# Kernel tuning notes

Hardware: AMD Instinct MI355X
Metric: run time of the kernel (lower is better)

Reference implementation:

```python
import jax, jax.numpy as jnp
import numpy as np

B, N, S, VC, P, E, H = 8, 1024, 64, 8, 3, 64, 4
HD = E // H


def setup_inputs() -> dict:
    key = jax.random.key(0)
    ks = jax.random.split(key, 20)
    def rn(k, shape, scale=1.0):
        return jax.random.normal(k, shape, dtype=jnp.float32) * scale
    inp = {
        "s": rn(ks[0], (B, N, S)),
        "v": rn(ks[1], (B, N, VC, 3)),
        "coords": rn(ks[2], (B, N, 3)),
        # p-adic encoder: Linear(1,16) -> SiLU -> Linear(16, 64)
        "enc_w1": rn(ks[3], (16, 1), 1.0),
        "enc_b1": jnp.zeros((16,), jnp.float32),
        "enc_w2": rn(ks[4], (S, 16), 1.0 / np.sqrt(16)),
        "enc_b2": jnp.zeros((S,), jnp.float32),
        # 3 GVP layers, all with s_cat dim 72 -> s_out 64, v 8 -> 8
        "scal_w": rn(ks[5], (3, S, S + VC), 1.0 / np.sqrt(S + VC)),
        "scal_b": jnp.zeros((3, S), jnp.float32),
        "vec_w": rn(ks[6], (3, VC, VC), 1.0 / np.sqrt(VC)),
        "gate_w": rn(ks[7], (3, VC, S + VC), 1.0 / np.sqrt(S + VC)),
        "gate_b": jnp.zeros((3, VC), jnp.float32),
        # MultiheadAttention (embed 64, 4 heads)
        "in_proj_w": rn(ks[8], (3 * E, E), 1.0 / np.sqrt(E)),
        "in_proj_b": jnp.zeros((3 * E,), jnp.float32),
        "out_proj_w": rn(ks[9], (E, E), 1.0 / np.sqrt(E)),
        "out_proj_b": jnp.zeros((E,), jnp.float32),
    }
    return inp


def _padic_distance(coords):
    # pairwise diffs (B, N, N, 3)
    diff = coords[:, :, None, :] - coords[:, None, :, :]
    di = (jnp.abs(diff) * 1000.0).astype(jnp.int32)
    # valuation = max k in [1,10] with p^k | di  == count of divisible k (divisibility chain)
    cnt = jnp.zeros(di.shape, jnp.int32)
    for k in range(1, 11):
        cnt = cnt + (di % (P ** k) == 0).astype(jnp.int32)
    val = jnp.where(di > 0, cnt, 0).astype(jnp.float32).mean(-1)  # (B,N,N)
    return jnp.float32(P) ** (-val)


def reference(s, v, coords, enc_w1, enc_b1, enc_w2, enc_b2,
              scal_w, scal_b, vec_w, gate_w, gate_b,
              in_proj_w, in_proj_b, out_proj_w, out_proj_b):
    silu = jax.nn.silu
    pd = _padic_distance(coords)  # (B,N,N)
    pf = silu(pd.mean(-1, keepdims=True) @ enc_w1.T + enc_b1) @ enc_w2.T + enc_b2
    s = s + pf

    for i in range(3):
        act = i < 2  # last layer has no activations (gate always applied)
        vn = jnp.linalg.norm(v, axis=-1)               # (B,N,VC)
        sc = jnp.concatenate([s, vn], axis=-1)         # (B,N,S+VC)
        s_new = sc @ scal_w[i].T + scal_b[i]
        if act:
            s_new = silu(s_new)
        v_new = jnp.einsum('oi,bnix->bnox', vec_w[i], v)
        if act:
            v_new = v_new * jax.nn.sigmoid(jnp.linalg.norm(v_new, axis=-1, keepdims=True))
        gate = jax.nn.sigmoid(sc @ gate_w[i].T + gate_b[i])
        v_new = v_new * gate[..., None]
        if i > 0:
            s, v = s + s_new, v + v_new
        else:
            s, v = s_new, v_new

    # p-adic biased multi-head attention (additive mask = -padic_dist per head)
    qkv = s @ in_proj_w.T + in_proj_b                 # (B,N,3E)
    q, k, vv = jnp.split(qkv, 3, axis=-1)
    q = q.reshape(B, N, H, HD)
    k = k.reshape(B, N, H, HD)
    vv = vv.reshape(B, N, H, HD)
    scores = jnp.einsum('bqhd,bkhd->bhqk', q, k) / np.sqrt(HD)
    scores = scores - pd[:, None, :, :]
    attn = jax.nn.softmax(scores, axis=-1)
    o = jnp.einsum('bhqk,bkhd->bqhd', attn, vv).reshape(B, N, E)
    s = s + (o @ out_proj_w.T + out_proj_b)

    return s, v, pd
```

## Files before the change

### kernel.cpp

```cpp
#include <hip/hip_runtime.h>
#include <hip/hip_bf16.h>
#include <math.h>

#define BB 8
#define NN 1024
#define SS 64
#define VCC 8
#define EE 64
#define HH 4
#define HDD 16

#define OUT_S_OFF 0
#define OUT_V_OFF 524288
#define OUT_PD_OFF 720896

__device__ __forceinline__ int val3(int d) {
    int c = 0;
    unsigned ud = (unsigned)d;
    c += (ud % 3u == 0u);
    c += (ud % 9u == 0u);
    c += (ud % 27u == 0u);
    c += (ud % 81u == 0u);
    c += (ud % 243u == 0u);
    c += (ud % 729u == 0u);
    c += (ud % 2187u == 0u);
    c += (ud % 6561u == 0u);
    c += (ud % 19683u == 0u);
    c += (ud % 59049u == 0u);
    return d > 0 ? c : 0;
}

__device__ __forceinline__ float silu_f(float x) {
    return x / (1.0f + expf(-x));
}
__device__ __forceinline__ float sigmoid_f(float x) {
    return 1.0f / (1.0f + expf(-x));
}

__global__ __launch_bounds__(256) void pd_kernel(const float* __restrict__ coords,
                                                 float* __restrict__ pd_out,
                                                 float* __restrict__ pdmean) {
    const int row = blockIdx.x;
    const int b = row >> 10;
    const int i = row & 1023;
    const int tid = threadIdx.x;
    const float* cb = coords + (size_t)b * NN * 3;

    __shared__ float sx[1024];
    __shared__ float sy[1024];
    __shared__ float sz[1024];
    __shared__ float red[4];

    for (int idx = tid; idx < 3072; idx += 256) {
        float v = cb[idx];
        int j = idx / 3;
        int c = idx - j * 3;
        float* dst = (c == 0) ? sx : (c == 1) ? sy : sz;
        dst[j] = v;
    }
    __syncthreads();

    const float cx = sx[i], cy = sy[i], cz = sz[i];
    float* prow = pd_out + (size_t)row * NN;
    const float kLog2_3_over3 = 0.5283208335737187f;

    const int j0 = tid * 4;
    float4 x4 = *(const float4*)&sx[j0];
    float4 y4 = *(const float4*)&sy[j0];
    float4 z4 = *(const float4*)&sz[j0];

    float p[4];
    float xs[4] = {x4.x, x4.y, x4.z, x4.w};
    float ys[4] = {y4.x, y4.y, y4.z, y4.w};
    float zs[4] = {z4.x, z4.y, z4.z, z4.w};
    float lsum = 0.0f;
    #pragma unroll
    for (int t = 0; t < 4; ++t) {
        int d0 = (int)(fabsf(cx - xs[t]) * 1000.0f);
        int d1 = (int)(fabsf(cy - ys[t]) * 1000.0f);
        int d2 = (int)(fabsf(cz - zs[t]) * 1000.0f);
        int cnt = val3(d0) + val3(d1) + val3(d2);
        p[t] = exp2f(-(float)cnt * kLog2_3_over3);
        lsum += p[t];
    }
    float4 pv = make_float4(p[0], p[1], p[2], p[3]);
    *(float4*)&prow[j0] = pv;

    float x = lsum;
    #pragma unroll
    for (int off = 32; off > 0; off >>= 1) x += __shfl_xor(x, off, 64);
    if ((tid & 63) == 0) red[tid >> 6] = x;
    __syncthreads();
    if (tid == 0) pdmean[row] = (red[0] + red[1] + red[2] + red[3]) * (1.0f / 1024.0f);
}

#define GR 4
__global__ __launch_bounds__(64) void gvp_kernel(const float* __restrict__ s_in,
                           const float* __restrict__ v_in,
                           const float* __restrict__ enc_w1,
                           const float* __restrict__ enc_b1,
                           const float* __restrict__ enc_w2,
                           const float* __restrict__ enc_b2,
                           const float* __restrict__ scal_w,
                           const float* __restrict__ scal_b,
                           const float* __restrict__ vec_w,
                           const float* __restrict__ gate_w,
                           const float* __restrict__ gate_b,
                           const float* __restrict__ pdmean,
                           float* __restrict__ s_gvp,
                           float* __restrict__ v_out) {
    const int lane = threadIdx.x;
    const int rbase = blockIdx.x * GR;

    __shared__ float sc[GR][80];
    __shared__ float vbuf[GR][24];
    __shared__ float vtb[GR][24];
    __shared__ float gg[GR][8];
    __shared__ float hid[GR][16];

    #pragma unroll
    for (int r = 0; r < GR; ++r) {
        const int row = rbase + r;
        sc[r][lane] = s_in[(size_t)row * 64 + lane];
        if (lane < 24) vbuf[r][lane] = v_in[(size_t)row * 24 + lane];
        if (lane < 16) {
            float pm = pdmean[row];
            hid[r][lane] = silu_f(pm * enc_w1[lane] + enc_b1[lane]);
        }
    }
    __syncthreads();
    #pragma unroll
    for (int r = 0; r < GR; ++r) {
        float acc = enc_b2[lane];
        #pragma unroll
        for (int h = 0; h < 16; ++h) acc += hid[r][h] * enc_w2[lane * 16 + h];
        sc[r][lane] += acc;
    }
    __syncthreads();

    for (int layer = 0; layer < 3; ++layer) {
        const bool act = layer < 2;
        if (lane < 8) {
            #pragma unroll
            for (int r = 0; r < GR; ++r) {
                float x = vbuf[r][lane * 3 + 0];
                float y = vbuf[r][lane * 3 + 1];
                float z = vbuf[r][lane * 3 + 2];
                sc[r][64 + lane] = sqrtf(x * x + y * y + z * z);
            }
        }
        __syncthreads();

        float sn[GR];
        {
            float4 w4[18];
            const float4* wr = (const float4*)(scal_w + ((size_t)layer * 64 + lane) * 72);
            #pragma unroll
            for (int k = 0; k < 18; ++k) w4[k] = wr[k];
            const float sb = scal_b[layer * 64 + lane];
            #pragma unroll
            for (int r = 0; r < GR; ++r) {
                const float4* sv = (const float4*)sc[r];
                float acc = sb;
                #pragma unroll
                for (int k = 0; k < 18; ++k) {
                    float4 s4 = sv[k];
                    acc += w4[k].x * s4.x + w4[k].y * s4.y + w4[k].z * s4.z + w4[k].w * s4.w;
                }
                sn[r] = acc;
            }
        }
        if (lane < 8) {
            float4 g4[18];
            const float4* gr_ = (const float4*)(gate_w + ((size_t)layer * 8 + lane) * 72);
            #pragma unroll
            for (int k = 0; k < 18; ++k) g4[k] = gr_[k];
            const float gb = gate_b[layer * 8 + lane];
            #pragma unroll
            for (int r = 0; r < GR; ++r) {
                const float4* sv = (const float4*)sc[r];
                float acc = gb;
                #pragma unroll
                for (int k = 0; k < 18; ++k) {
                    float4 s4 = sv[k];
                    acc += g4[k].x * s4.x + g4[k].y * s4.y + g4[k].z * s4.z + g4[k].w * s4.w;
                }
                gg[r][lane] = sigmoid_f(acc);
            }
        }
        if (lane < 24) {
            const int o = lane / 3;
            const int xc = lane - o * 3;
            const float* vw = vec_w + ((size_t)layer * 8 + o) * 8;
            float vwr[8];
            #pragma unroll
            for (int ii = 0; ii < 8; ++ii) vwr[ii] = vw[ii];
            #pragma unroll
            for (int r = 0; r < GR; ++r) {
                float acc = 0.0f;
                #pragma unroll
                for (int ii = 0; ii < 8; ++ii) acc += vwr[ii] * vbuf[r][ii * 3 + xc];
                vtb[r][lane] = acc;
            }
        }
        __syncthreads();

        #pragma unroll
        for (int r = 0; r < GR; ++r) {
            float val = act ? silu_f(sn[r]) : sn[r];
            sc[r][lane] = (layer > 0) ? (sc[r][lane] + val) : val;
        }
        if (lane < 24) {
            const int o = lane / 3;
            #pragma unroll
            for (int r = 0; r < GR; ++r) {
                float val = vtb[r][lane];
                if (act) {
                    float a = vtb[r][o * 3 + 0];
                    float bb2 = vtb[r][o * 3 + 1];
                    float c2 = vtb[r][o * 3 + 2];
                    val *= sigmoid_f(sqrtf(a * a + bb2 * bb2 + c2 * c2));
                }
                val *= gg[r][o];
                vbuf[r][lane] = (layer > 0) ? (vbuf[r][lane] + val) : val;
            }
        }
        __syncthreads();
    }

    #pragma unroll
    for (int r = 0; r < GR; ++r) {
        const int row = rbase + r;
        s_gvp[(size_t)row * 64 + lane] = sc[r][lane];
        if (lane < 24) v_out[(size_t)row * 24 + lane] = vbuf[r][lane];
    }
}

#define QROWS 8
__global__ __launch_bounds__(192) void qkv_kernel(const float* __restrict__ s_gvp,
                           const float* __restrict__ w,
                           const float* __restrict__ bias,
                           float* __restrict__ q,
                           float* __restrict__ k,
                           float* __restrict__ v) {
    const int tid = threadIdx.x;
    const int rbase = blockIdx.x * QROWS;
    __shared__ float sl[QROWS][64];
    for (int idx = tid; idx < QROWS * 64; idx += 192)
        sl[idx >> 6][idx & 63] = s_gvp[(size_t)rbase * 64 + idx];
    __syncthreads();

    float4 w4[16];
    const float4* wr = (const float4*)(w + (size_t)tid * 64);
    #pragma unroll
    for (int kk = 0; kk < 16; ++kk) w4[kk] = wr[kk];
    const float bv = bias[tid];

    const int which = tid >> 6;
    const int e = tid & 63;
    const int h = e >> 4, d = e & 15;
    float* dst = (which == 0) ? q : (which == 1) ? k : v;

    #pragma unroll
    for (int r = 0; r < QROWS; ++r) {
        const float4* sv = (const float4*)sl[r];
        float acc = bv;
        #pragma unroll
        for (int kk = 0; kk < 16; ++kk) {
            float4 s4 = sv[kk];
            acc += w4[kk].x * s4.x + w4[kk].y * s4.y + w4[kk].z * s4.z + w4[kk].w * s4.w;
        }
        const int row = rbase + r;
        const int b = row >> 10, n = row & 1023;
        dst[(((size_t)(b * HH + h)) * NN + n) * HDD + d] = acc;
    }
}

__global__ __launch_bounds__(256, 2)
void attn_kernel(const float* __restrict__ q,
                 const float* __restrict__ k,
                 const float* __restrict__ v,
                 const float* __restrict__ pd,
                 float* __restrict__ o) {
    const int bh = blockIdx.x >> 5;
    const int qt = blockIdx.x & 31;
    const int b = bh >> 2;
    const int h = bh & 3;
    const int tid = threadIdx.x;
    const int kl = tid & 15;
    const int qg = tid >> 4;
    const int qbase = qt * 32 + qg * 2;

    __shared__ float kt[128][20];
    __shared__ float vt[128][20];

    float qreg[2][16];
    const float* qb_ = q + ((size_t)bh * NN + qbase) * HDD;
    #pragma unroll
    for (int i = 0; i < 2; ++i) {
        #pragma unroll
        for (int d = 0; d < 16; d += 4) {
            float4 t4 = *(const float4*)(qb_ + i * 16 + d);
            qreg[i][d] = t4.x; qreg[i][d+1] = t4.y; qreg[i][d+2] = t4.z; qreg[i][d+3] = t4.w;
        }
    }
    const float* pdr0 = pd + ((size_t)b * NN + qbase) * NN;

    float acc[2][16];
    #pragma unroll
    for (int i = 0; i < 2; ++i)
        #pragma unroll
        for (int d = 0; d < 16; ++d) acc[i][d] = 0.0f;
    float mrun[2] = {-INFINITY, -INFINITY};
    float lrun[2] = {0.0f, 0.0f};

    const float* kbase = k + (size_t)bh * NN * HDD;
    const float* vbase = v + (size_t)bh * NN * HDD;
    const float kLog2e = 1.44269504f;

    for (int tile = 0; tile < 8; ++tile) {
        __syncthreads();
        {
            const float4* kg = (const float4*)(kbase + (size_t)tile * 128 * 16);
            const float4* vg = (const float4*)(vbase + (size_t)tile * 128 * 16);
            int c0 = tid, c1 = tid + 256;
            int r0 = c0 >> 2, s0 = c0 & 3;
            int r1 = c1 >> 2, s1 = c1 & 3;
            *(float4*)&kt[r0][s0 * 4] = kg[c0];
            *(float4*)&kt[r1][s1 * 4] = kg[c1];
            *(float4*)&vt[r0][s0 * 4] = vg[c0];
            *(float4*)&vt[r1][s1 * 4] = vg[c1];
        }
        __syncthreads();

        float sc[2][8];
        #pragma unroll
        for (int m = 0; m < 8; ++m) {
            const int jt = kl + 16 * m;
            float kr[16];
            #pragma unroll
            for (int d = 0; d < 16; d += 4) {
                float4 t4 = *(const float4*)&kt[jt][d];
                kr[d] = t4.x; kr[d+1] = t4.y; kr[d+2] = t4.z; kr[d+3] = t4.w;
            }
            const int j = tile * 128 + jt;
            #pragma unroll
            for (int i = 0; i < 2; ++i) {
                float a = 0.0f;
                #pragma unroll
                for (int d = 0; d < 16; ++d) a += qreg[i][d] * kr[d];
                sc[i][m] = a * 0.25f - pdr0[(size_t)i * NN + j];
            }
        }

        #pragma unroll
        for (int i = 0; i < 2; ++i) {
            float tmax = sc[i][0];
            #pragma unroll
            for (int m = 1; m < 8; ++m) tmax = fmaxf(tmax, sc[i][m]);
            #pragma unroll
            for (int w = 1; w < 16; w <<= 1) tmax = fmaxf(tmax, __shfl_xor(tmax, w, 16));
            float mnew = fmaxf(mrun[i], tmax);
            float scale = exp2f((mrun[i] - mnew) * kLog2e);
            mrun[i] = mnew;
            lrun[i] *= scale;
            #pragma unroll
            for (int d = 0; d < 16; ++d) acc[i][d] *= scale;
            float ls = 0.0f;
            #pragma unroll
            for (int m = 0; m < 8; ++m) {
                float p = exp2f((sc[i][m] - mnew) * kLog2e);
                sc[i][m] = p;
                ls += p;
            }
            lrun[i] += ls;
        }

        #pragma unroll
        for (int m = 0; m < 8; ++m) {
            const int jt = kl + 16 * m;
            float vr[16];
            #pragma unroll
            for (int d = 0; d < 16; d += 4) {
                float4 t4 = *(const float4*)&vt[jt][d];
                vr[d] = t4.x; vr[d+1] = t4.y; vr[d+2] = t4.z; vr[d+3] = t4.w;
            }
            #pragma unroll
            for (int i = 0; i < 2; ++i) {
                const float p = sc[i][m];
                #pragma unroll
                for (int d = 0; d < 16; ++d) acc[i][d] += p * vr[d];
            }
        }
    }

    #pragma unroll
    for (int i = 0; i < 2; ++i) {
        float l = lrun[i];
        #pragma unroll
        for (int w = 1; w < 16; w <<= 1) l += __shfl_xor(l, w, 16);
        lrun[i] = l;
    }
    float outv[2] = {0.0f, 0.0f};
    #pragma unroll
    for (int i = 0; i < 2; ++i) {
        #pragma unroll
        for (int d = 0; d < 16; ++d) {
            float a = acc[i][d];
            #pragma unroll
            for (int w = 1; w < 16; w <<= 1) a += __shfl_xor(a, w, 16);
            if (kl == d) outv[i] = a;
        }
    }
    #pragma unroll
    for (int i = 0; i < 2; ++i) {
        const int qi = qbase + i;
        o[((size_t)(b * NN + qi)) * EE + h * HDD + kl] = outv[i] / lrun[i];
    }
}

#define OROWS 16
__global__ __launch_bounds__(256) void outproj_kernel(const float* __restrict__ s_gvp,
                               const float* __restrict__ o,
                               const float* __restrict__ w,
                               const float* __restrict__ bias,
                               float* __restrict__ s_out) {
    const int tid = threadIdx.x;
    const int col = tid & 63;
    const int wq = tid >> 6;
    const int rbase = blockIdx.x * OROWS;
    __shared__ float ol[OROWS][64];
    for (int idx = tid; idx < OROWS * 64; idx += 256)
        ol[idx >> 6][idx & 63] = o[(size_t)rbase * 64 + idx];
    __syncthreads();

    float4 w4[16];
    const float4* wr = (const float4*)(w + (size_t)col * 64);
    #pragma unroll
    for (int kk = 0; kk < 16; ++kk) w4[kk] = wr[kk];
    const float bv = bias[col];

    #pragma unroll
    for (int rr = 0; rr < OROWS / 4; ++rr) {
        const int r = wq * (OROWS / 4) + rr;
        const float4* sv = (const float4*)ol[r];
        float acc = bv;
        #pragma unroll
        for (int kk = 0; kk < 16; ++kk) {
            float4 s4 = sv[kk];
            acc += w4[kk].x * s4.x + w4[kk].y * s4.y + w4[kk].z * s4.z + w4[kk].w * s4.w;
        }
        const int row = rbase + r;
        s_out[(size_t)row * 64 + col] = s_gvp[(size_t)row * 64 + col] + acc;
    }
}

extern "C" void kernel_launch(void* const* d_in, const int* in_sizes, int n_in,
                              void* d_out, int out_size, void* d_ws, size_t ws_size,
                              hipStream_t stream) {
    const float* s_in      = (const float*)d_in[0];
    const float* v_in      = (const float*)d_in[1];
    const float* coords    = (const float*)d_in[2];
    const float* enc_w1    = (const float*)d_in[3];
    const float* enc_b1    = (const float*)d_in[4];
    const float* enc_w2    = (const float*)d_in[5];
    const float* enc_b2    = (const float*)d_in[6];
    const float* scal_w    = (const float*)d_in[7];
    const float* scal_b    = (const float*)d_in[8];
    const float* vec_w     = (const float*)d_in[9];
    const float* gate_w    = (const float*)d_in[10];
    const float* gate_b    = (const float*)d_in[11];
    const float* in_proj_w = (const float*)d_in[12];
    const float* in_proj_b = (const float*)d_in[13];
    const float* out_proj_w= (const float*)d_in[14];
    const float* out_proj_b= (const float*)d_in[15];

    float* out_s  = (float*)d_out + OUT_S_OFF;
    float* out_v  = (float*)d_out + OUT_V_OFF;
    float* out_pd = (float*)d_out + OUT_PD_OFF;

    float* ws      = (float*)d_ws;
    float* pdmean  = ws;
    float* s_gvp   = ws + 8192;
    float* qb      = s_gvp + 524288;
    float* kb      = qb + 524288;
    float* vvb     = kb + 524288;
    float* ob      = vvb + 524288;

    const int rows = BB * NN;

    pd_kernel<<<rows, 256, 0, stream>>>(coords, out_pd, pdmean);
    gvp_kernel<<<rows / GR, 64, 0, stream>>>(s_in, v_in, enc_w1, enc_b1, enc_w2, enc_b2,
                                             scal_w, scal_b, vec_w, gate_w, gate_b,
                                             pdmean, s_gvp, out_v);
    qkv_kernel<<<rows / QROWS, 192, 0, stream>>>(s_gvp, in_proj_w, in_proj_b, qb, kb, vvb);
    attn_kernel<<<BB * HH * (NN / 32), 256, 0, stream>>>(qb, kb, vvb, out_pd, ob);
    outproj_kernel<<<rows / OROWS, 256, 0, stream>>>(s_gvp, ob, out_proj_w, out_proj_b, out_s);
}
```

Baseline: 212.7 us.

## Split attention over key halves, merge partials in outproj, batch pd rows per block

The attention kernel now handles 4 query rows per thread and splits the key range into two halves across blocks. Each block writes partial outputs plus running max and sum, and the output-projection kernel merges the two halves with a log-sum-exp combine. The pd kernel now computes 16 rows per block, so the coordinate staging into shared memory happens once per block instead of once per row. The goal is better reuse of the K/V tiles loaded into shared memory and less per-block overhead, at the cost of more registers per thread, extra workspace for the partials, and merge work in outproj.

```diff
diff --git a/kernel.cpp b/kernel.cpp
--- a/kernel.cpp
+++ b/kernel.cpp
@@ -37,19 +37,20 @@
     return 1.0f / (1.0f + expf(-x));
 }
 
+#define IR 16
 __global__ __launch_bounds__(256) void pd_kernel(const float* __restrict__ coords,
                                                  float* __restrict__ pd_out,
                                                  float* __restrict__ pdmean) {
-    const int row = blockIdx.x;
-    const int b = row >> 10;
-    const int i = row & 1023;
+    const int bi = blockIdx.x;
+    const int b = bi >> 6;
+    const int ibase = (bi & 63) * IR;
     const int tid = threadIdx.x;
     const float* cb = coords + (size_t)b * NN * 3;
 
     __shared__ float sx[1024];
     __shared__ float sy[1024];
     __shared__ float sz[1024];
-    __shared__ float red[4];
+    __shared__ float red[IR][4];
 
     for (int idx = tid; idx < 3072; idx += 256) {
         float v = cb[idx];
@@ -60,38 +61,42 @@
     }
     __syncthreads();
 
-    const float cx = sx[i], cy = sy[i], cz = sz[i];
-    float* prow = pd_out + (size_t)row * NN;
-    const float kLog2_3_over3 = 0.5283208335737187f;
-
     const int j0 = tid * 4;
     float4 x4 = *(const float4*)&sx[j0];
     float4 y4 = *(const float4*)&sy[j0];
     float4 z4 = *(const float4*)&sz[j0];
-
-    float p[4];
     float xs[4] = {x4.x, x4.y, x4.z, x4.w};
     float ys[4] = {y4.x, y4.y, y4.z, y4.w};
     float zs[4] = {z4.x, z4.y, z4.z, z4.w};
-    float lsum = 0.0f;
-    #pragma unroll
-    for (int t = 0; t < 4; ++t) {
-        int d0 = (int)(fabsf(cx - xs[t]) * 1000.0f);
-        int d1 = (int)(fabsf(cy - ys[t]) * 1000.0f);
-        int d2 = (int)(fabsf(cz - zs[t]) * 1000.0f);
-        int cnt = val3(d0) + val3(d1) + val3(d2);
-        p[t] = exp2f(-(float)cnt * kLog2_3_over3);
-        lsum += p[t];
-    }
-    float4 pv = make_float4(p[0], p[1], p[2], p[3]);
-    *(float4*)&prow[j0] = pv;
-
-    float x = lsum;
-    #pragma unroll
-    for (int off = 32; off > 0; off >>= 1) x += __shfl_xor(x, off, 64);
-    if ((tid & 63) == 0) red[tid >> 6] = x;
+
+    const float kLog2_3_over3 = 0.5283208335737187f;
+
+    for (int ii = 0; ii < IR; ++ii) {
+        const int i = ibase + ii;
+        const float cx = sx[i], cy = sy[i], cz = sz[i];
+        float p[4];
+        float lsum = 0.0f;
+        #pragma unroll
+        for (int t = 0; t < 4; ++t) {
+            int d0 = (int)(fabsf(cx - xs[t]) * 1000.0f);
+            int d1 = (int)(fabsf(cy - ys[t]) * 1000.0f);
+            int d2 = (int)(fabsf(cz - zs[t]) * 1000.0f);
+            int cnt = val3(d0) + val3(d1) + val3(d2);
+            p[t] = exp2f(-(float)cnt * kLog2_3_over3);
+            lsum += p[t];
+        }
+        *(float4*)&pd_out[((size_t)(b * NN + i)) * NN + j0] =
+            make_float4(p[0], p[1], p[2], p[3]);
+        float x = lsum;
+        #pragma unroll
+        for (int off = 32; off > 0; off >>= 1) x += __shfl_xor(x, off, 64);
+        if ((tid & 63) == 0) red[ii][tid >> 6] = x;
+    }
     __syncthreads();
-    if (tid == 0) pdmean[row] = (red[0] + red[1] + red[2] + red[3]) * (1.0f / 1024.0f);
+    if (tid < IR) {
+        pdmean[b * NN + ibase + tid] =
+            (red[tid][0] + red[tid][1] + red[tid][2] + red[tid][3]) * (1.0f / 1024.0f);
+    }
 }
 
 #define GR 4
@@ -276,49 +281,51 @@
     }
 }
 
-__global__ __launch_bounds__(256, 2)
+__global__ __launch_bounds__(256, 4)
 void attn_kernel(const float* __restrict__ q,
                  const float* __restrict__ k,
                  const float* __restrict__ v,
                  const float* __restrict__ pd,
-                 float* __restrict__ o) {
+                 float* __restrict__ po,
+                 float* __restrict__ pm,
+                 float* __restrict__ pl) {
+    const int ks = blockIdx.x & 1;
+    const int qt = (blockIdx.x >> 1) & 15;
     const int bh = blockIdx.x >> 5;
-    const int qt = blockIdx.x & 31;
     const int b = bh >> 2;
-    const int h = bh & 3;
     const int tid = threadIdx.x;
     const int kl = tid & 15;
     const int qg = tid >> 4;
-    const int qbase = qt * 32 + qg * 2;
+    const int qbase = qt * 64 + qg * 4;
 
     __shared__ float kt[128][20];
     __shared__ float vt[128][20];
 
-    float qreg[2][16];
+    float qreg[4][16];
     const float* qb_ = q + ((size_t)bh * NN + qbase) * HDD;
     #pragma unroll
-    for (int i = 0; i < 2; ++i) {
+    for (int i = 0; i < 4; ++i) {
         #pragma unroll
         for (int d = 0; d < 16; d += 4) {
             float4 t4 = *(const float4*)(qb_ + i * 16 + d);
             qreg[i][d] = t4.x; qreg[i][d+1] = t4.y; qreg[i][d+2] = t4.z; qreg[i][d+3] = t4.w;
         }
     }
-    const float* pdr0 = pd + ((size_t)b * NN + qbase) * NN;
-
-    float acc[2][16];
-    #pragma unroll
-    for (int i = 0; i < 2; ++i)
+    const float* pdr0 = pd + ((size_t)b * NN + qbase) * NN + ks * 512;
+
+    float acc[4][16];
+    #pragma unroll
+    for (int i = 0; i < 4; ++i)
         #pragma unroll
         for (int d = 0; d < 16; ++d) acc[i][d] = 0.0f;
-    float mrun[2] = {-INFINITY, -INFINITY};
-    float lrun[2] = {0.0f, 0.0f};
-
-    const float* kbase = k + (size_t)bh * NN * HDD;
-    const float* vbase = v + (size_t)bh * NN * HDD;
+    float mrun[4] = {-INFINITY, -INFINITY, -INFINITY, -INFINITY};
+    float lrun[4] = {0.0f, 0.0f, 0.0f, 0.0f};
+
+    const float* kbase = k + ((size_t)bh * NN + ks * 512) * HDD;
+    const float* vbase = v + ((size_t)bh * NN + ks * 512) * HDD;
     const float kLog2e = 1.44269504f;
 
-    for (int tile = 0; tile < 8; ++tile) {
+    for (int tile = 0; tile < 4; ++tile) {
         __syncthreads();
         {
             const float4* kg = (const float4*)(kbase + (size_t)tile * 128 * 16);
@@ -333,7 +340,7 @@
         }
         __syncthreads();
 
-        float sc[2][8];
+        float sc[4][8];
         #pragma unroll
         for (int m = 0; m < 8; ++m) {
             const int jt = kl + 16 * m;
@@ -345,7 +352,7 @@
             }
             const int j = tile * 128 + jt;
             #pragma unroll
-            for (int i = 0; i < 2; ++i) {
+            for (int i = 0; i < 4; ++i) {
                 float a = 0.0f;
                 #pragma unroll
                 for (int d = 0; d < 16; ++d) a += qreg[i][d] * kr[d];
@@ -354,7 +361,7 @@
         }
 
         #pragma unroll
-        for (int i = 0; i < 2; ++i) {
+        for (int i = 0; i < 4; ++i) {
             float tmax = sc[i][0];
             #pragma unroll
             for (int m = 1; m < 8; ++m) tmax = fmaxf(tmax, sc[i][m]);
@@ -386,7 +393,7 @@
                 vr[d] = t4.x; vr[d+1] = t4.y; vr[d+2] = t4.z; vr[d+3] = t4.w;
             }
             #pragma unroll
-            for (int i = 0; i < 2; ++i) {
+            for (int i = 0; i < 4; ++i) {
                 const float p = sc[i][m];
                 #pragma unroll
                 for (int d = 0; d < 16; ++d) acc[i][d] += p * vr[d];
@@ -395,15 +402,15 @@
     }
 
     #pragma unroll
-    for (int i = 0; i < 2; ++i) {
+    for (int i = 0; i < 4; ++i) {
         float l = lrun[i];
         #pragma unroll
         for (int w = 1; w < 16; w <<= 1) l += __shfl_xor(l, w, 16);
         lrun[i] = l;
     }
-    float outv[2] = {0.0f, 0.0f};
-    #pragma unroll
-    for (int i = 0; i < 2; ++i) {
+    float outv[4] = {0.0f, 0.0f, 0.0f, 0.0f};
+    #pragma unroll
+    for (int i = 0; i < 4; ++i) {
         #pragma unroll
         for (int d = 0; d < 16; ++d) {
             float a = acc[i][d];
@@ -412,16 +419,22 @@
             if (kl == d) outv[i] = a;
         }
     }
-    #pragma unroll
-    for (int i = 0; i < 2; ++i) {
-        const int qi = qbase + i;
-        o[((size_t)(b * NN + qi)) * EE + h * HDD + kl] = outv[i] / lrun[i];
+    const size_t sbase = (size_t)ks * 32768 + (size_t)bh * NN + qbase;
+    #pragma unroll
+    for (int i = 0; i < 4; ++i) {
+        po[(sbase + i) * 16 + kl] = outv[i];
+        if (kl == 0) {
+            pm[sbase + i] = mrun[i];
+            pl[sbase + i] = lrun[i];
+        }
     }
 }
 
 #define OROWS 16
 __global__ __launch_bounds__(256) void outproj_kernel(const float* __restrict__ s_gvp,
-                               const float* __restrict__ o,
+                               const float* __restrict__ po,
+                               const float* __restrict__ pm,
+                               const float* __restrict__ pl,
                                const float* __restrict__ w,
                                const float* __restrict__ bias,
                                float* __restrict__ s_out) {
@@ -430,8 +443,22 @@
     const int wq = tid >> 6;
     const int rbase = blockIdx.x * OROWS;
     __shared__ float ol[OROWS][64];
-    for (int idx = tid; idx < OROWS * 64; idx += 256)
-        ol[idx >> 6][idx & 63] = o[(size_t)rbase * 64 + idx];
+    const float kLog2e = 1.44269504f;
+    for (int idx = tid; idx < OROWS * 64; idx += 256) {
+        const int r = idx >> 6;
+        const int c = idx & 63;
+        const int row = rbase + r;
+        const int b = row >> 10, n = row & 1023;
+        const int h = c >> 4, d = c & 15;
+        const size_t i2 = (size_t)(b * HH + h) * NN + n;
+        float m0 = pm[i2], m1 = pm[32768 + i2];
+        float l0 = pl[i2], l1 = pl[32768 + i2];
+        float a0 = po[i2 * 16 + d], a1 = po[(32768 + i2) * 16 + d];
+        float mm = fmaxf(m0, m1);
+        float e0 = exp2f((m0 - mm) * kLog2e);
+        float e1 = exp2f((m1 - mm) * kLog2e);
+        ol[r][c] = (a0 * e0 + a1 * e1) / (l0 * e0 + l1 * e1);
+    }
     __syncthreads();
 
     float4 w4[16];
@@ -485,15 +512,18 @@
     float* qb      = s_gvp + 524288;
     float* kb      = qb + 524288;
     float* vvb     = kb + 524288;
-    float* ob      = vvb + 524288;
+    float* po      = vvb + 524288;
+    float* pm      = po + 2 * 32768 * 16;
+    float* pl      = pm + 2 * 32768;
 
     const int rows = BB * NN;
 
-    pd_kernel<<<rows, 256, 0, stream>>>(coords, out_pd, pdmean);
+    pd_kernel<<<BB * (NN / IR), 256, 0, stream>>>(coords, out_pd, pdmean);
     gvp_kernel<<<rows / GR, 64, 0, stream>>>(s_in, v_in, enc_w1, enc_b1, enc_w2, enc_b2,
                                              scal_w, scal_b, vec_w, gate_w, gate_b,
                                              pdmean, s_gvp, out_v);
     qkv_kernel<<<rows / QROWS, 192, 0, stream>>>(s_gvp, in_proj_w, in_proj_b, qb, kb, vvb);
-    attn_kernel<<<BB * HH * (NN / 32), 256, 0, stream>>>(qb, kb, vvb, out_pd, ob);
-    outproj_kernel<<<rows / OROWS, 256, 0, stream>>>(s_gvp, ob, out_proj_w, out_proj_b, out_s);
-}
+    attn_kernel<<<BB * HH * (NN / 64) * 2, 256, 0, stream>>>(qb, kb, vvb, out_pd, po, pm, pl);
+    outproj_kernel<<<rows / OROWS, 256, 0, stream>>>(s_gvp, po, pm, pl,
+                                                     out_proj_w, out_proj_b, out_s);
+}
```

Result: slower. 334.7 us (+57.4%).
